# Kernel optimization log

Hardware: AMD Instinct MI355X
Metric: run time of the kernel (lower is better)

## Reference

```python
import jax, jax.numpy as jnp
import numpy as np

KS = 7
ITERS = 6
B, C, H, W = 2, 64, 256, 1216

_WM7 = [1,1,1,1,1,1,1,1,0,0,0,0,0,1,1,0,0,0,0,0,1,1,0,0,0,0,0,1,1,0,0,0,0,0,1,1,0,0,0,0,0,1,1,1,1,1,1,1,1]
_WM5 = [0,0,0,0,0,0,0,0,1,1,1,1,1,0,0,1,0,0,0,1,0,0,1,0,0,0,1,0,0,1,0,0,0,1,0,0,1,1,1,1,1,0,0,0,0,0,0,0,0]
_WM3 = [0,0,0,0,0,0,0,0,0,0,0,0,0,0,0,0,1,1,1,0,0,0,0,1,0,1,0,0,0,0,1,1,1,0,0,0,0,0,0,0,0,0,0,0,0,0,0,0,0]

# per 7x7 position t: which guide tensor (ring) and which channel within it
_SRC = []
_i7 = _i5 = _i3 = 0
for _t in range(KS * KS):
    if _WM7[_t]:
        _SRC.append(("7", _i7)); _i7 += 1
    elif _WM5[_t]:
        _SRC.append(("5", _i5)); _i5 += 1
    elif _WM3[_t]:
        _SRC.append(("3", _i3)); _i3 += 1
    else:
        _SRC.append(("1", 0))


def _convbn(x, w, s, b):
    # Conv2d(bias=False) + BatchNorm2d (inference) folded to per-channel scale/bias.
    y = jax.lax.conv_general_dilated(x, w, window_strides=(1, 1),
                                     padding=((1, 1), (1, 1)),
                                     dimension_numbers=("NCHW", "OIHW", "NCHW"))
    return y * s[None, :, None, None] + b[None, :, None, None]


def setup_inputs() -> dict:
    key = jax.random.key(0)
    ks = iter(jax.random.split(key, 64))
    def nrm(shape, scale=1.0):
        return jax.random.normal(next(ks), shape, jnp.float32) * scale
    def uni(shape):
        return jax.random.uniform(next(ks), shape, dtype=jnp.float32)
    inp = {
        "feature": nrm((B, C, H, W)),
        "d0": uni((B, 1, H, W)),
        "d00": nrm((B, 1, H, W)),  # ~half positive -> mixed valid_mask
    }
    layers = [("aff7", 24), ("aff5", 16), ("aff3", 8),
              ("att7", 6), ("att5", 6), ("att3", 6), ("att1", 6), ("mask", 6)]
    fan = 1.0 / np.sqrt(C * 9)
    for name, out in layers:
        inp["w_" + name] = nrm((out, C, 3, 3), fan)
        inp["s_" + name] = uni((out,))
        inp["b_" + name] = nrm((out,), 0.1)
    return inp


def reference(feature, d0, d00,
              w_aff7, s_aff7, b_aff7, w_aff5, s_aff5, b_aff5, w_aff3, s_aff3, b_aff3,
              w_att7, s_att7, b_att7, w_att5, s_att5, b_att5, w_att3, s_att3, b_att3,
              w_att1, s_att1, b_att1, w_mask, s_mask, b_mask):
    valid = (d00 > 0).astype(d00.dtype)
    mask_all = jax.nn.sigmoid(_convbn(feature, w_mask, s_mask, b_mask)) * valid
    aff7 = _convbn(feature, w_aff7, s_aff7, b_aff7)  # [B,24,H,W]
    aff5 = _convbn(feature, w_aff5, s_aff5, b_aff5)  # [B,16,H,W]
    aff3 = _convbn(feature, w_aff3, s_aff3, b_aff3)  # [B, 8,H,W]
    att7 = jax.nn.sigmoid(_convbn(feature, w_att7, s_att7, b_att7))
    att5 = jax.nn.sigmoid(_convbn(feature, w_att5, s_att5, b_att5))
    att3 = jax.nn.sigmoid(_convbn(feature, w_att3, s_att3, b_att3))
    att1 = jax.nn.sigmoid(_convbn(feature, w_att1, s_att1, b_att1))

    dt = d0
    for it in range(ITERS):
        mask = mask_all[:, it:it + 1]
        g7 = att7[:, it:it + 1] * aff7
        g5 = att5[:, it:it + 1] * aff5
        g3 = att3[:, it:it + 1] * aff3
        g1 = att1[:, it:it + 1]
        denom = (jnp.sum(jnp.abs(g7), 1, keepdims=True)
                 + jnp.sum(jnp.abs(g5), 1, keepdims=True)
                 + jnp.sum(jnp.abs(g3), 1, keepdims=True)
                 + jnp.abs(g1))
        g7, g5, g3, g1 = g7 / denom, g5 / denom, g3 / denom, g1 / denom
        g0 = 1.0 - (jnp.sum(g7, 1, keepdims=True) + jnp.sum(g5, 1, keepdims=True)
                    + jnp.sum(g3, 1, keepdims=True) + g1)
        guides = {"7": g7, "5": g5, "3": g3, "1": g1}
        # scatter ring guides into full 49-channel 7x7 layout
        G = jnp.concatenate([guides[k][:, i:i + 1] for k, i in _SRC], axis=1)  # [B,49,H,W]
        # weighted neighbor gather: out(p) = sum_t G_t(p+off_t) * dt(p+off_t)
        P = G * dt  # [B,49,H,W]
        Pp = jnp.pad(P, ((0, 0), (0, 0), (3, 3), (3, 3)))
        acc = jnp.zeros_like(dt)
        for t in range(KS * KS):
            i, j = t // KS, t % KS
            acc = acc + Pp[:, t:t + 1, 6 - i:6 - i + H, 6 - j:6 - j + W]
        dt = acc + g0 * d0
        dt = mask * d00 + (1.0 - mask) * dt
    return dt
```

## Files before the change

kernel.cpp:

```cpp
#include <hip/hip_runtime.h>
#include <hip/hip_fp16.h>
#include <stdint.h>

#define HH 256
#define WW 1216
#define BB 2
#define CC 64
#define IPIX (HH*WW)
#define NPIX (BB*IPIX)
#define PW 1280
#define PH 262
#define PPIX (PH*PW)
#define PLSTRIDE (BB*PPIX)
#define XOFF 32

typedef __attribute__((ext_vector_type(8))) __bf16 bf16x8;
typedef __attribute__((ext_vector_type(4))) __bf16 bf16x4;
typedef __attribute__((ext_vector_type(4))) float floatx4;
typedef __attribute__((ext_vector_type(4))) _Float16 half4;

__device__ __forceinline__ float sigm(float x) { return 1.f / (1.f + __expf(-x)); }

constexpr int LSTART_H[9] = {0,24,40,48,54,60,66,72,78};

constexpr int PLANE[49] = {
  0, 1, 2, 3, 4, 5, 6,
  7,24,25,26,27,28, 8,
  9,29,40,41,42,30,10,
 11,31,43,-1,44,32,12,
 13,33,45,46,47,34,14,
 15,35,36,37,38,39,16,
 17,18,19,20,21,22,23};
constexpr int KCLS[49] = {
 0,0,0,0,0,0,0,
 0,1,1,1,1,1,0,
 0,1,2,2,2,1,0,
 0,1,2,3,2,1,0,
 0,1,2,2,2,1,0,
 0,1,1,1,1,1,0,
 0,0,0,0,0,0,0};
constexpr int TAPNC[48] = {
  0,1,2,3,4,5,6,7,8,9,10,11,12,13,14,15,16,17,18,19,20,21,22,23,
  25,26,27,28,29,30,31,32,33,34,35,36,37,38,39,40,41,42,43,44,45,46,47,48};

struct WPtrs {
    const float* w[8];
    const float* s[8];
    const float* b[8];
};

__global__ void k_pack(WPtrs wp, __bf16* __restrict__ wpk,
                       float* __restrict__ s_all, float* __restrict__ b_all) {
    int idx = blockIdx.x * blockDim.x + threadIdx.x;
    if (idx < 18 * 5 * 64) {
        int kk = idx / (5 * 64);
        int r = idx - kk * 5 * 64;
        int t = r >> 6, lane = r & 63;
        int m = t * 16 + (lane & 15);
        int L = 0, o = 0;
        bool valid_m = (m < 78);
        if (valid_m) {
            for (int i = 0; i < 8; i++) if (m >= LSTART_H[i]) { L = i; o = m - LSTART_H[i]; }
        }
        __bf16 vals[8];
        for (int j = 0; j < 8; j++) {
            int k = kk * 32 + ((lane >> 4) * 8) + j;
            int tap = k >> 6, c = k & 63;
            float w = valid_m ? wp.w[L][(o * 64 + c) * 9 + tap] : 0.f;
            vals[j] = (__bf16)w;
        }
        for (int j = 0; j < 8; j++) wpk[(size_t)idx * 8 + j] = vals[j];
    }
    if (idx < 80) {
        int m = idx;
        float sv = 0.f, bv = 0.f;
        if (m < 78) {
            int L = 0, o = 0;
            for (int i = 0; i < 8; i++) if (m >= LSTART_H[i]) { L = i; o = m - LSTART_H[i]; }
            sv = wp.s[L][o]; bv = wp.b[L][o];
        }
        s_all[m] = sv; b_all[m] = bv;
    }
}

__global__ void k_zero_pad(__bf16* __restrict__ aff_p) {
    const int perPB = 6 * PW + 256 * 16;
    int idx = blockIdx.x * blockDim.x + threadIdx.x;
    int total = 48 * BB * perPB;
    if (idx >= total) return;
    int pbi = idx / perPB;
    int e = idx - pbi * perPB;
    int plane = pbi >> 1, b = pbi & 1;
    int r, c;
    if (e < 6 * PW) {
        int rr = e / PW; c = e - rr * PW;
        r = (rr < 3) ? rr : (259 + rr - 3);
    } else {
        int j = e - 6 * PW;
        r = 3 + (j >> 4);
        int c16 = j & 15;
        c = (c16 < 8) ? (24 + c16) : (1248 + c16 - 8);
    }
    aff_p[(size_t)plane * PLSTRIDE + (size_t)b * PPIX + r * PW + c] = (__bf16)0.f;
}

__global__ __launch_bounds__(256) void k_cvt(const float* __restrict__ feat,
                                             __bf16* __restrict__ fpk) {
    const int x = blockIdx.x * 64 + (threadIdx.x & 63);
    const int half = threadIdx.x >> 6;
    const int y = blockIdx.y, b = blockIdx.z;
    const float* fb = feat + (size_t)b * CC * IPIX + (size_t)y * WW + x;
    __bf16* op = fpk + ((size_t)(b * IPIX + y * WW + x) << 6);
#pragma unroll
    for (int h = 0; h < 2; h++) {
        const int cg = half + h * 4;
        bf16x8 pk;
#pragma unroll
        for (int j = 0; j < 8; j++) pk[j] = (__bf16)fb[(size_t)(cg * 8 + j) * IPIX];
        *(bf16x8*)(op + cg * 8) = pk;
    }
}

__global__ __launch_bounds__(256, 4) void k_conv(const __bf16* __restrict__ fpk,
        const float* __restrict__ d00, const __bf16* __restrict__ wpk,
        const float* __restrict__ s_all, const float* __restrict__ b_all,
        __bf16* __restrict__ aff_p, __bf16* __restrict__ attp, __bf16* __restrict__ maskp,
        float* __restrict__ stp) {
    __shared__ __bf16 sh[6 * 34 * 72];
    __shared__ __bf16 wlds[2 * 2560];
    const int tid = threadIdx.x;
    int flat = blockIdx.x + 38 * (blockIdx.y + 64 * blockIdx.z);
    int nf = (flat & 7) * 608 + (flat >> 3);
    int bx = nf % 38; int r2 = nf / 38;
    const int x0 = bx * 32, y0 = (r2 & 63) * 4, b = r2 >> 6;

    {
        bf16x8 w0 = *(const bf16x8*)(wpk + (size_t)tid * 8);
        *(bf16x8*)(wlds + tid * 8) = w0;
        if (tid < 64) {
            bf16x8 w1 = *(const bf16x8*)(wpk + 2048 + (size_t)tid * 8);
            *(bf16x8*)(wlds + 2048 + tid * 8) = w1;
        }
    }
    for (int idx = tid; idx < 204 * 8; idx += 256) {
        int cg = idx & 7, pos = idx >> 3;
        int row = pos / 34, x = pos - row * 34;
        int gy = y0 + row - 1, gx = x0 + x - 1;
        bf16x8 pk;
#pragma unroll
        for (int j = 0; j < 8; j++) pk[j] = (__bf16)0.f;
        if (gy >= 0 && gy < HH && gx >= 0 && gx < WW)
            pk = *(const bf16x8*)(fpk + ((size_t)(b * IPIX + gy * WW + gx) << 6) + cg * 8);
        *(bf16x8*)(sh + pos * 72 + cg * 8) = pk;
    }
    __syncthreads();

    const int wave = tid >> 6, lane = tid & 63;
    const int n = lane & 15, g = lane >> 4;

    floatx4 acc[5][2];
#pragma unroll
    for (int t = 0; t < 5; t++)
#pragma unroll
        for (int q = 0; q < 2; q++) acc[t][q] = (floatx4)(0.f);

#pragma unroll
    for (int kk = 0; kk < 18; kk++) {
        bf16x8 wt0, wt1;
        if (kk < 17) {
            wt0 = *(const bf16x8*)(wpk + (size_t)(kk + 1) * 2560 + tid * 8);
            if (tid < 64) wt1 = *(const bf16x8*)(wpk + (size_t)(kk + 1) * 2560 + 2048 + tid * 8);
        }
        const int tap = kk >> 1;
        const int dy = tap / 3 - 1, dx = tap % 3 - 1;
        const int c0 = (kk & 1) * 32 + g * 8;
        bf16x8 bfr[2];
        const int rowb = wave + 1 + dy;
        const int colb = 1 + dx + n;
#pragma unroll
        for (int q = 0; q < 2; q++)
            bfr[q] = *(const bf16x8*)(sh + ((rowb * 34) + colb + q * 16) * 72 + c0);
        bf16x8 afr[5];
        const __bf16* wb = wlds + (kk & 1) * 2560 + lane * 8;
#pragma unroll
        for (int t = 0; t < 5; t++) afr[t] = *(const bf16x8*)(wb + t * 512);
#pragma unroll
        for (int t = 0; t < 5; t++)
#pragma unroll
            for (int q = 0; q < 2; q++)
                acc[t][q] = __builtin_amdgcn_mfma_f32_16x16x32_bf16(afr[t], bfr[q], acc[t][q], 0, 0, 0);
        if (kk < 17) {
            *(bf16x8*)(wlds + ((kk + 1) & 1) * 2560 + tid * 8) = wt0;
            if (tid < 64) *(bf16x8*)(wlds + ((kk + 1) & 1) * 2560 + 2048 + tid * 8) = wt1;
        }
        __syncthreads();
    }

    const int pix_base = b * IPIX + (y0 + wave) * WW + x0 + n;
    float p7[2] = {0,0}, t7[2] = {0,0};
    float p5[2] = {0,0}, t5[2] = {0,0};
    float p3[2] = {0,0}, t3[2] = {0,0};

#pragma unroll
    for (int t = 0; t < 5; t++) {
        const floatx4 sv = *(const floatx4*)(s_all + t * 16 + 4 * g);
        const floatx4 bv = *(const floatx4*)(b_all + t * 16 + 4 * g);
#pragma unroll
        for (int q = 0; q < 2; q++) {
#pragma unroll
            for (int reg = 0; reg < 4; reg++) {
                const int m = t * 16 + 4 * g + reg;
                const float v = fmaf(acc[t][q][reg], sv[reg], bv[reg]);
                if (m < 24)                { p7[q] += fabsf(v); t7[q] += v; }
                else if (m < 40)           { p5[q] += fabsf(v); t5[q] += v; }
                else if (m < 48)           { p3[q] += fabsf(v); t3[q] += v; }
                const float outv = (m < 48) ? v : sigm(v);
                sh[m * 132 + wave * 32 + n + q * 16] = (__bf16)outv;
            }
        }
    }
#pragma unroll
    for (int q = 0; q < 2; q++) {
        p7[q] += __shfl_xor(p7[q], 16); p7[q] += __shfl_xor(p7[q], 32);
        t7[q] += __shfl_xor(t7[q], 16); t7[q] += __shfl_xor(t7[q], 32);
        p5[q] += __shfl_xor(p5[q], 16); p5[q] += __shfl_xor(p5[q], 32);
        t5[q] += __shfl_xor(t5[q], 16); t5[q] += __shfl_xor(t5[q], 32);
        p3[q] += __shfl_xor(p3[q], 16); p3[q] += __shfl_xor(p3[q], 32);
        t3[q] += __shfl_xor(t3[q], 16); t3[q] += __shfl_xor(t3[q], 32);
    }
    if (g == 0) {
#pragma unroll
        for (int q = 0; q < 2; q++) {
            const int pixq = pix_base + q * 16;
            floatx4 s0 = {p7[q], p5[q], p3[q], t7[q]};
            floatx4 s1 = {t5[q], t3[q], 0.f, 0.f};
            *(floatx4*)(stp + (size_t)pixq * 8)     = s0;
            *(floatx4*)(stp + (size_t)pixq * 8 + 4) = s1;
        }
    }
    __syncthreads();

    const int px = tid & 127;
    const int grp = tid >> 7;
    const int prow = px >> 5, pcol = px & 31;
    const size_t ppx = (size_t)b * PPIX + (y0 + prow + 3) * PW + (x0 + pcol + XOFF);
    const int pix = b * IPIX + (y0 + prow) * WW + x0 + pcol;
#pragma unroll
    for (int m = 0; m < 48; m += 2) {
        aff_p[(size_t)(m + grp) * PLSTRIDE + ppx] = sh[(m + grp) * 132 + px];
    }
    const float d00v = d00[pix];
    const float valid = (d00v > 0.f) ? 1.f : 0.f;
#pragma unroll
    for (int j = 0; j < 6; j += 2) {
        const int it = j + grp;
        bf16x4 av = { sh[(48 + it) * 132 + px], sh[(54 + it) * 132 + px],
                      sh[(60 + it) * 132 + px], sh[(66 + it) * 132 + px] };
        *(bf16x4*)(attp + ((size_t)it * NPIX + pix) * 4) = av;
        maskp[(size_t)it * NPIX + pix] = (__bf16)((float)sh[(72 + it) * 132 + px] * valid);
    }
}

__global__ __launch_bounds__(256) void k_rg(const __bf16* __restrict__ attp,
        const float* __restrict__ stp, const float* __restrict__ d0,
        _Float16* __restrict__ rp, float* __restrict__ gd) {
    int g = blockIdx.x * blockDim.x + threadIdx.x;
    if (g >= NPIX) return;
    const floatx4 s0 = *(const floatx4*)(stp + (size_t)g * 8);
    const floatx4 s1 = *(const floatx4*)(stp + (size_t)g * 8 + 4);
    const float S7 = s0[0], S5 = s0[1], S3 = s0[2], T7 = s0[3], T5 = s1[0], T3 = s1[1];
    const float d0v = d0[g];
#pragma unroll
    for (int it = 0; it < 6; it++) {
        bf16x4 a = *(const bf16x4*)(attp + ((size_t)it * NPIX + g) * 4);
        float a7 = (float)a[0], a5 = (float)a[1], a3 = (float)a[2], a1 = (float)a[3];
        float denom = a7 * S7 + a5 * S5 + a3 * S3 + a1;
        float inv = 1.f / denom;
        float r7 = a7 * inv, r5 = a5 * inv, r3 = a3 * inv, r1 = a1 * inv;
        float g0 = 1.f - (r7 * T7 + r5 * T5 + r3 * T3 + r1);
        half4 rv = {(_Float16)r7, (_Float16)r5, (_Float16)r3, (_Float16)r1};
        *(half4*)(rp + ((size_t)it * NPIX + g) * 4) = rv;
        gd[(size_t)it * NPIX + g] = g0 * d0v;
    }
}

__global__ __launch_bounds__(256) void k_iter(const _Float16* __restrict__ rp,
        const float* __restrict__ gd, const float* __restrict__ dt,
        const __bf16* __restrict__ aff_p, const __bf16* __restrict__ maskp,
        const float* __restrict__ d00,
        float* __restrict__ dtn, int it) {
    __shared__ float sp[5][14 * 38];
    const int tid = threadIdx.x;
    const int tx = tid & 31, ty = tid >> 5;
    int flat = blockIdx.x + 38 * (blockIdx.y + 32 * blockIdx.z);
    int nf = (flat & 7) * 304 + (flat >> 3);
    int bx = nf % 38; int r2 = nf / 38;
    const int x0 = bx * 32, y0 = (r2 & 31) * 8, b = r2 >> 5;
    const int ib = b * IPIX;

    for (int idx = tid; idx < 14 * 38; idx += 256) {
        int r = idx / 38, col = idx - r * 38;
        int gy = y0 + r - 3, gx = x0 + col - 3;
        float v7 = 0.f, v5 = 0.f, v3 = 0.f, v1 = 0.f, vb = 0.f;
        if (gy >= 0 && gy < HH && gx >= 0 && gx < WW) {
            int q = ib + gy * WW + gx;
            half4 rv = *(const half4*)(rp + ((size_t)it * NPIX + q) * 4);
            float dtv = dt[q];
            v7 = (float)rv[0] * dtv; v5 = (float)rv[1] * dtv;
            v3 = (float)rv[2] * dtv; v1 = (float)rv[3] * dtv;
            vb = gd[(size_t)it * NPIX + q];
        }
        sp[0][idx] = v7; sp[1][idx] = v5; sp[2][idx] = v3; sp[3][idx] = v1; sp[4][idx] = vb;
    }
    __syncthreads();

    const int y = y0 + ty, x = x0 + tx;
    const int pix = ib + y * WW + x;
    const __bf16* ap = aff_p + (size_t)b * PPIX + (y + 3) * PW + (x + XOFF);

    float acc0 = sp[4][(ty + 3) * 38 + (tx + 3)] + sp[3][(ty + 3) * 38 + (tx + 3)];
    float acc1 = 0.f, acc2 = 0.f, acc3 = 0.f;
#pragma unroll
    for (int bt = 0; bt < 6; bt++) {
        float a8[8];
#pragma unroll
        for (int j = 0; j < 8; j++) {
            const int t = TAPNC[bt * 8 + j];
            const int dy = 3 - t / 7, dx = 3 - (t % 7);
            a8[j] = (float)ap[(ptrdiff_t)PLANE[t] * PLSTRIDE + dy * PW + dx];
        }
#pragma unroll
        for (int j = 0; j < 8; j++) {
            const int t = TAPNC[bt * 8 + j];
            const int dy = 3 - t / 7, dx = 3 - (t % 7);
            const float pv = sp[KCLS[t]][(ty + dy + 3) * 38 + (tx + dx + 3)];
            switch (j & 3) {
                case 0: acc0 = fmaf(a8[j], pv, acc0); break;
                case 1: acc1 = fmaf(a8[j], pv, acc1); break;
                case 2: acc2 = fmaf(a8[j], pv, acc2); break;
                default: acc3 = fmaf(a8[j], pv, acc3); break;
            }
        }
    }
    float acc = (acc0 + acc1) + (acc2 + acc3);
    float m = (float)maskp[(size_t)it * NPIX + pix];
    float dtv = m * d00[pix] + (1.f - m) * acc;
    dtn[pix] = dtv;
}

extern "C" void kernel_launch(void* const* d_in, const int* in_sizes, int n_in,
                              void* d_out, int out_size, void* d_ws, size_t ws_size,
                              hipStream_t stream) {
    const float* feat = (const float*)d_in[0];
    const float* d0   = (const float*)d_in[1];
    const float* d00  = (const float*)d_in[2];
    WPtrs wp;
    for (int l = 0; l < 8; l++) {
        wp.w[l] = (const float*)d_in[3 + 3 * l];
        wp.s[l] = (const float*)d_in[4 + 3 * l];
        wp.b[l] = (const float*)d_in[5 + 3 * l];
    }
    __bf16*   wsb   = (__bf16*)d_ws;
    __bf16*   aff_p = wsb;
    __bf16*   attp  = aff_p + (size_t)48 * PLSTRIDE;
    __bf16*   msk_b = attp + (size_t)24 * NPIX;
    float*    stp   = (float*)(msk_b + (size_t)6 * NPIX);
    float*    dtA   = stp + (size_t)8 * NPIX;
    __bf16*   wpk   = (__bf16*)(dtA + (size_t)NPIX);
    float*    s_all = (float*)(wpk + 18 * 5 * 64 * 8);
    float*    b_all = s_all + 80;
    char*     X     = (char*)(b_all + 80);
    __bf16*   fpk   = (__bf16*)X;
    _Float16* rp    = (_Float16*)X;
    float*    gd    = (float*)(X + (size_t)24 * NPIX * 2);
    float*    dtB   = (float*)d_out;

    hipLaunchKernelGGL(k_pack, dim3(23), dim3(256), 0, stream, wp, wpk, s_all, b_all);
    hipLaunchKernelGGL(k_zero_pad, dim3((48 * BB * (6 * PW + 256 * 16) + 255) / 256), dim3(256),
                       0, stream, aff_p);
    hipLaunchKernelGGL(k_cvt, dim3(WW / 64, HH, BB), dim3(256), 0, stream, feat, fpk);
    hipLaunchKernelGGL(k_conv, dim3(38, 64, 2), dim3(256), 0, stream,
                       fpk, d00, wpk, s_all, b_all, aff_p, attp, msk_b, stp);
    hipLaunchKernelGGL(k_rg, dim3(NPIX / 256), dim3(256), 0, stream,
                       attp, stp, d0, rp, gd);
    const float* cur = d0;
    for (int it = 0; it < 6; ++it) {
        float* nxt = (it & 1) ? dtB : dtA;
        if (it == 5) nxt = dtB;
        hipLaunchKernelGGL(k_iter, dim3(38, 32, 2), dim3(256), 0, stream,
                           rp, gd, cur, aff_p, msk_b, d00, nxt, it);
        cur = nxt;
    }
}
```

Baseline: 523.6 us.

## Store affinities pixel-major and scatter iteration taps via LDS atomics

The 48 affinity planes are now written in a pixel-interleaved layout (48 bf16 per pixel) instead of padded planar buffers, so the zero-pad kernel goes away. The iteration kernel changes from a gather to a scatter: each source pixel reads its 48 contiguous affinities and atomically adds the weighted contributions into an LDS accumulation tile, on a taller 16-row tile. The conv kernel drops its LDS double-buffered weight staging and per-step barriers, reading weights directly from global/L2, and raises its occupancy hint. The trade-offs are heavy LDS atomic traffic (49 atomics per source pixel, with halo redundancy) and weight loads that now go to cache instead of LDS.

```diff
diff --git a/kernel.cpp b/kernel.cpp
--- a/kernel.cpp
+++ b/kernel.cpp
@@ -8,11 +8,6 @@
 #define CC 64
 #define IPIX (HH*WW)
 #define NPIX (BB*IPIX)
-#define PW 1280
-#define PH 262
-#define PPIX (PH*PW)
-#define PLSTRIDE (BB*PPIX)
-#define XOFF 32
 
 typedef __attribute__((ext_vector_type(8))) __bf16 bf16x8;
 typedef __attribute__((ext_vector_type(4))) __bf16 bf16x4;
@@ -49,6 +44,10 @@
     const float* b[8];
 };
 
+__device__ __forceinline__ void lds_fadd(float* p, float v) {
+    __hip_atomic_fetch_add(p, v, __ATOMIC_RELAXED, __HIP_MEMORY_SCOPE_WORKGROUP);
+}
+
 __global__ void k_pack(WPtrs wp, __bf16* __restrict__ wpk,
                        float* __restrict__ s_all, float* __restrict__ b_all) {
     int idx = blockIdx.x * blockDim.x + threadIdx.x;
@@ -83,27 +82,6 @@
     }
 }
 
-__global__ void k_zero_pad(__bf16* __restrict__ aff_p) {
-    const int perPB = 6 * PW + 256 * 16;
-    int idx = blockIdx.x * blockDim.x + threadIdx.x;
-    int total = 48 * BB * perPB;
-    if (idx >= total) return;
-    int pbi = idx / perPB;
-    int e = idx - pbi * perPB;
-    int plane = pbi >> 1, b = pbi & 1;
-    int r, c;
-    if (e < 6 * PW) {
-        int rr = e / PW; c = e - rr * PW;
-        r = (rr < 3) ? rr : (259 + rr - 3);
-    } else {
-        int j = e - 6 * PW;
-        r = 3 + (j >> 4);
-        int c16 = j & 15;
-        c = (c16 < 8) ? (24 + c16) : (1248 + c16 - 8);
-    }
-    aff_p[(size_t)plane * PLSTRIDE + (size_t)b * PPIX + r * PW + c] = (__bf16)0.f;
-}
-
 __global__ __launch_bounds__(256) void k_cvt(const float* __restrict__ feat,
                                              __bf16* __restrict__ fpk) {
     const int x = blockIdx.x * 64 + (threadIdx.x & 63);
@@ -121,27 +99,18 @@
     }
 }
 
-__global__ __launch_bounds__(256, 4) void k_conv(const __bf16* __restrict__ fpk,
+__global__ __launch_bounds__(256, 5) void k_conv(const __bf16* __restrict__ fpk,
         const float* __restrict__ d00, const __bf16* __restrict__ wpk,
         const float* __restrict__ s_all, const float* __restrict__ b_all,
-        __bf16* __restrict__ aff_p, __bf16* __restrict__ attp, __bf16* __restrict__ maskp,
+        __bf16* __restrict__ afx, __bf16* __restrict__ attp, __bf16* __restrict__ maskp,
         float* __restrict__ stp) {
     __shared__ __bf16 sh[6 * 34 * 72];
-    __shared__ __bf16 wlds[2 * 2560];
     const int tid = threadIdx.x;
     int flat = blockIdx.x + 38 * (blockIdx.y + 64 * blockIdx.z);
     int nf = (flat & 7) * 608 + (flat >> 3);
     int bx = nf % 38; int r2 = nf / 38;
     const int x0 = bx * 32, y0 = (r2 & 63) * 4, b = r2 >> 6;
 
-    {
-        bf16x8 w0 = *(const bf16x8*)(wpk + (size_t)tid * 8);
-        *(bf16x8*)(wlds + tid * 8) = w0;
-        if (tid < 64) {
-            bf16x8 w1 = *(const bf16x8*)(wpk + 2048 + (size_t)tid * 8);
-            *(bf16x8*)(wlds + 2048 + tid * 8) = w1;
-        }
-    }
     for (int idx = tid; idx < 204 * 8; idx += 256) {
         int cg = idx & 7, pos = idx >> 3;
         int row = pos / 34, x = pos - row * 34;
@@ -166,11 +135,6 @@
 
 #pragma unroll
     for (int kk = 0; kk < 18; kk++) {
-        bf16x8 wt0, wt1;
-        if (kk < 17) {
-            wt0 = *(const bf16x8*)(wpk + (size_t)(kk + 1) * 2560 + tid * 8);
-            if (tid < 64) wt1 = *(const bf16x8*)(wpk + (size_t)(kk + 1) * 2560 + 2048 + tid * 8);
-        }
         const int tap = kk >> 1;
         const int dy = tap / 3 - 1, dx = tap % 3 - 1;
         const int c0 = (kk & 1) * 32 + g * 8;
@@ -180,8 +144,8 @@
 #pragma unroll
         for (int q = 0; q < 2; q++)
             bfr[q] = *(const bf16x8*)(sh + ((rowb * 34) + colb + q * 16) * 72 + c0);
+        const __bf16* wb = wpk + (size_t)kk * 2560 + lane * 8;
         bf16x8 afr[5];
-        const __bf16* wb = wlds + (kk & 1) * 2560 + lane * 8;
 #pragma unroll
         for (int t = 0; t < 5; t++) afr[t] = *(const bf16x8*)(wb + t * 512);
 #pragma unroll
@@ -189,12 +153,8 @@
 #pragma unroll
             for (int q = 0; q < 2; q++)
                 acc[t][q] = __builtin_amdgcn_mfma_f32_16x16x32_bf16(afr[t], bfr[q], acc[t][q], 0, 0, 0);
-        if (kk < 17) {
-            *(bf16x8*)(wlds + ((kk + 1) & 1) * 2560 + tid * 8) = wt0;
-            if (tid < 64) *(bf16x8*)(wlds + ((kk + 1) & 1) * 2560 + 2048 + tid * 8) = wt1;
-        }
-        __syncthreads();
-    }
+    }
+    __syncthreads();
 
     const int pix_base = b * IPIX + (y0 + wave) * WW + x0 + n;
     float p7[2] = {0,0}, t7[2] = {0,0};
@@ -240,15 +200,27 @@
     }
     __syncthreads();
 
+    {
+        const int pxi = tid >> 1;
+        const int hf = tid & 1;
+        const int prow2 = pxi >> 5, pcol2 = pxi & 31;
+        const int pix2 = b * IPIX + (y0 + prow2) * WW + x0 + pcol2;
+#pragma unroll
+        for (int k = 0; k < 3; k++) {
+            bf16x8 v;
+#pragma unroll
+            for (int e = 0; e < 8; e++) {
+                const int jj = hf * 24 + k * 8 + e;
+                v[e] = sh[PLANE[TAPNC[jj]] * 132 + pxi];
+            }
+            *(bf16x8*)(afx + (size_t)pix2 * 48 + hf * 24 + k * 8) = v;
+        }
+    }
+
     const int px = tid & 127;
     const int grp = tid >> 7;
     const int prow = px >> 5, pcol = px & 31;
-    const size_t ppx = (size_t)b * PPIX + (y0 + prow + 3) * PW + (x0 + pcol + XOFF);
     const int pix = b * IPIX + (y0 + prow) * WW + x0 + pcol;
-#pragma unroll
-    for (int m = 0; m < 48; m += 2) {
-        aff_p[(size_t)(m + grp) * PLSTRIDE + ppx] = sh[(m + grp) * 132 + px];
-    }
     const float d00v = d00[pix];
     const float valid = (d00v > 0.f) ? 1.f : 0.f;
 #pragma unroll
@@ -286,66 +258,67 @@
 
 __global__ __launch_bounds__(256) void k_iter(const _Float16* __restrict__ rp,
         const float* __restrict__ gd, const float* __restrict__ dt,
-        const __bf16* __restrict__ aff_p, const __bf16* __restrict__ maskp,
+        const __bf16* __restrict__ afx, const __bf16* __restrict__ maskp,
         const float* __restrict__ d00,
         float* __restrict__ dtn, int it) {
-    __shared__ float sp[5][14 * 38];
+    __shared__ float accs[28 * 44];
     const int tid = threadIdx.x;
+    int flat = blockIdx.x + 38 * (blockIdx.y + 16 * blockIdx.z);
+    int nf = (flat & 7) * 152 + (flat >> 3);
+    int bx = nf % 38; int r2 = nf / 38;
+    const int x0 = bx * 32, y0 = (r2 & 15) * 16, b = r2 >> 4;
+    const int ib = b * IPIX;
+
+    for (int idx = tid; idx < 28 * 44; idx += 256) accs[idx] = 0.f;
+    __syncthreads();
+
+    for (int idx = tid; idx < 22 * 38; idx += 256) {
+        const int ly = idx / 38, lx = idx - ly * 38;
+        const int gy = y0 + ly - 3, gx = x0 + lx - 3;
+        if (gy >= 0 && gy < HH && gx >= 0 && gx < WW) {
+            const int q = ib + gy * WW + gx;
+            const half4 rv = *(const half4*)(rp + ((size_t)it * NPIX + q) * 4);
+            const float dtv = dt[q];
+            const float gdv = gd[(size_t)it * NPIX + q];
+            float rc[4];
+            rc[0] = (float)rv[0] * dtv; rc[1] = (float)rv[1] * dtv;
+            rc[2] = (float)rv[2] * dtv; rc[3] = (float)rv[3] * dtv;
+            bf16x8 A0 = *(const bf16x8*)(afx + (size_t)q * 48);
+            bf16x8 A1 = *(const bf16x8*)(afx + (size_t)q * 48 + 8);
+            bf16x8 A2 = *(const bf16x8*)(afx + (size_t)q * 48 + 16);
+            bf16x8 A3 = *(const bf16x8*)(afx + (size_t)q * 48 + 24);
+            bf16x8 A4 = *(const bf16x8*)(afx + (size_t)q * 48 + 32);
+            bf16x8 A5 = *(const bf16x8*)(afx + (size_t)q * 48 + 40);
+            float* abase = accs + ly * 44 + lx;
+            lds_fadd(abase + 3 * 44 + 3, rc[3] + gdv);
+#pragma unroll
+            for (int jj = 0; jj < 48; jj++) {
+                const int t = TAPNC[jj];
+                const int i = t / 7, j = t % 7;
+                float av;
+                switch (jj >> 3) {
+                    case 0: av = (float)A0[jj & 7]; break;
+                    case 1: av = (float)A1[jj & 7]; break;
+                    case 2: av = (float)A2[jj & 7]; break;
+                    case 3: av = (float)A3[jj & 7]; break;
+                    case 4: av = (float)A4[jj & 7]; break;
+                    default: av = (float)A5[jj & 7]; break;
+                }
+                lds_fadd(abase + i * 44 + j, av * rc[KCLS[t]]);
+            }
+        }
+    }
+    __syncthreads();
+
     const int tx = tid & 31, ty = tid >> 5;
-    int flat = blockIdx.x + 38 * (blockIdx.y + 32 * blockIdx.z);
-    int nf = (flat & 7) * 304 + (flat >> 3);
-    int bx = nf % 38; int r2 = nf / 38;
-    const int x0 = bx * 32, y0 = (r2 & 31) * 8, b = r2 >> 5;
-    const int ib = b * IPIX;
-
-    for (int idx = tid; idx < 14 * 38; idx += 256) {
-        int r = idx / 38, col = idx - r * 38;
-        int gy = y0 + r - 3, gx = x0 + col - 3;
-        float v7 = 0.f, v5 = 0.f, v3 = 0.f, v1 = 0.f, vb = 0.f;
-        if (gy >= 0 && gy < HH && gx >= 0 && gx < WW) {
-            int q = ib + gy * WW + gx;
-            half4 rv = *(const half4*)(rp + ((size_t)it * NPIX + q) * 4);
-            float dtv = dt[q];
-            v7 = (float)rv[0] * dtv; v5 = (float)rv[1] * dtv;
-            v3 = (float)rv[2] * dtv; v1 = (float)rv[3] * dtv;
-            vb = gd[(size_t)it * NPIX + q];
-        }
-        sp[0][idx] = v7; sp[1][idx] = v5; sp[2][idx] = v3; sp[3][idx] = v1; sp[4][idx] = vb;
-    }
-    __syncthreads();
-
-    const int y = y0 + ty, x = x0 + tx;
-    const int pix = ib + y * WW + x;
-    const __bf16* ap = aff_p + (size_t)b * PPIX + (y + 3) * PW + (x + XOFF);
-
-    float acc0 = sp[4][(ty + 3) * 38 + (tx + 3)] + sp[3][(ty + 3) * 38 + (tx + 3)];
-    float acc1 = 0.f, acc2 = 0.f, acc3 = 0.f;
-#pragma unroll
-    for (int bt = 0; bt < 6; bt++) {
-        float a8[8];
-#pragma unroll
-        for (int j = 0; j < 8; j++) {
-            const int t = TAPNC[bt * 8 + j];
-            const int dy = 3 - t / 7, dx = 3 - (t % 7);
-            a8[j] = (float)ap[(ptrdiff_t)PLANE[t] * PLSTRIDE + dy * PW + dx];
-        }
-#pragma unroll
-        for (int j = 0; j < 8; j++) {
-            const int t = TAPNC[bt * 8 + j];
-            const int dy = 3 - t / 7, dx = 3 - (t % 7);
-            const float pv = sp[KCLS[t]][(ty + dy + 3) * 38 + (tx + dx + 3)];
-            switch (j & 3) {
-                case 0: acc0 = fmaf(a8[j], pv, acc0); break;
-                case 1: acc1 = fmaf(a8[j], pv, acc1); break;
-                case 2: acc2 = fmaf(a8[j], pv, acc2); break;
-                default: acc3 = fmaf(a8[j], pv, acc3); break;
-            }
-        }
-    }
-    float acc = (acc0 + acc1) + (acc2 + acc3);
-    float m = (float)maskp[(size_t)it * NPIX + pix];
-    float dtv = m * d00[pix] + (1.f - m) * acc;
-    dtn[pix] = dtv;
+#pragma unroll
+    for (int r = 0; r < 16; r += 8) {
+        const int oy = ty + r;
+        const int pix = ib + (y0 + oy) * WW + (x0 + tx);
+        const float acc = accs[(oy + 6) * 44 + (tx + 6)];
+        const float m = (float)maskp[(size_t)it * NPIX + pix];
+        dtn[pix] = m * d00[pix] + (1.f - m) * acc;
+    }
 }
 
 extern "C" void kernel_launch(void* const* d_in, const int* in_sizes, int n_in,
@@ -361,8 +334,8 @@
         wp.b[l] = (const float*)d_in[5 + 3 * l];
     }
     __bf16*   wsb   = (__bf16*)d_ws;
-    __bf16*   aff_p = wsb;
-    __bf16*   attp  = aff_p + (size_t)48 * PLSTRIDE;
+    __bf16*   afx   = wsb;
+    __bf16*   attp  = afx + (size_t)48 * NPIX;
     __bf16*   msk_b = attp + (size_t)24 * NPIX;
     float*    stp   = (float*)(msk_b + (size_t)6 * NPIX);
     float*    dtA   = stp + (size_t)8 * NPIX;
@@ -376,19 +349,17 @@
     float*    dtB   = (float*)d_out;
 
     hipLaunchKernelGGL(k_pack, dim3(23), dim3(256), 0, stream, wp, wpk, s_all, b_all);
-    hipLaunchKernelGGL(k_zero_pad, dim3((48 * BB * (6 * PW + 256 * 16) + 255) / 256), dim3(256),
-                       0, stream, aff_p);
     hipLaunchKernelGGL(k_cvt, dim3(WW / 64, HH, BB), dim3(256), 0, stream, feat, fpk);
     hipLaunchKernelGGL(k_conv, dim3(38, 64, 2), dim3(256), 0, stream,
-                       fpk, d00, wpk, s_all, b_all, aff_p, attp, msk_b, stp);
+                       fpk, d00, wpk, s_all, b_all, afx, attp, msk_b, stp);
     hipLaunchKernelGGL(k_rg, dim3(NPIX / 256), dim3(256), 0, stream,
                        attp, stp, d0, rp, gd);
     const float* cur = d0;
     for (int it = 0; it < 6; ++it) {
         float* nxt = (it & 1) ? dtB : dtA;
         if (it == 5) nxt = dtB;
-        hipLaunchKernelGGL(k_iter, dim3(38, 32, 2), dim3(256), 0, stream,
-                           rp, gd, cur, aff_p, msk_b, d00, nxt, it);
+        hipLaunchKernelGGL(k_iter, dim3(38, 16, 2), dim3(256), 0, stream,
+                           rp, gd, cur, afx, msk_b, d00, nxt, it);
         cur = nxt;
     }
 }
```

Result: slower. 1.997 ms (+281.4%).

## Fuse pairs of propagation iterations into one kernel with halo recompute

Applied to the files above, without the earlier changes.

Replaces six per-iteration launches with three launches that each run two propagation steps. A wider halo of the weighted input is staged in shared memory, and the intermediate iteration is recomputed over a 22x38 region held in LDS, so the intermediate depth never goes to global memory. Tiles grow to 16 rows, and the gd term is folded into the fourth plane so there are four planes instead of five. The cost is redundant halo compute and extra affinity loads for the intermediate region, plus more shared memory per block, which may lower occupancy.

```diff
diff --git a/kernel.cpp b/kernel.cpp
--- a/kernel.cpp
+++ b/kernel.cpp
@@ -284,68 +284,121 @@
     }
 }
 
-__global__ __launch_bounds__(256) void k_iter(const _Float16* __restrict__ rp,
-        const float* __restrict__ gd, const float* __restrict__ dt,
+#define R0W 44
+#define R0N (28 * 44)
+#define R1W 38
+#define R1N (22 * 38)
+__global__ __launch_bounds__(256) void k_iter2(const _Float16* __restrict__ rp,
+        const float* __restrict__ gd, const float* __restrict__ src,
         const __bf16* __restrict__ aff_p, const __bf16* __restrict__ maskp,
         const float* __restrict__ d00,
-        float* __restrict__ dtn, int it) {
-    __shared__ float sp[5][14 * 38];
+        float* __restrict__ dtn, int itA) {
+    __shared__ float P0[4][R0N];
+    __shared__ float P1[4][R1N];
+    const int itB = itA + 1;
     const int tid = threadIdx.x;
+    int flat = blockIdx.x + 38 * (blockIdx.y + 16 * blockIdx.z);
+    int nf = (flat & 7) * 152 + (flat >> 3);
+    int bx = nf % 38; int r2 = nf / 38;
+    const int x0 = bx * 32, y0 = (r2 & 15) * 16, b = r2 >> 4;
+    const int ib = b * IPIX;
+
+    for (int idx = tid; idx < R0N; idx += 256) {
+        const int r = idx / R0W, c = idx - r * R0W;
+        const int gy = y0 + r - 6, gx = x0 + c - 6;
+        float c0 = 0.f, c1 = 0.f, c2 = 0.f, c3 = 0.f;
+        if (gy >= 0 && gy < HH && gx >= 0 && gx < WW) {
+            const int q = ib + gy * WW + gx;
+            const half4 rv = *(const half4*)(rp + ((size_t)itA * NPIX + q) * 4);
+            const float dtv = src[q];
+            const float gdv = gd[(size_t)itA * NPIX + q];
+            c0 = (float)rv[0] * dtv; c1 = (float)rv[1] * dtv;
+            c2 = (float)rv[2] * dtv; c3 = (float)rv[3] * dtv + gdv;
+        }
+        P0[0][idx] = c0; P0[1][idx] = c1; P0[2][idx] = c2; P0[3][idx] = c3;
+    }
+    __syncthreads();
+
+    for (int idx = tid; idx < R1N; idx += 256) {
+        const int r = idx / R1W, c = idx - r * R1W;
+        const int gy = y0 + r - 3, gx = x0 + c - 3;
+        float o0 = 0.f, o1 = 0.f, o2 = 0.f, o3 = 0.f;
+        if (gy >= 0 && gy < HH && gx >= 0 && gx < WW) {
+            const int q = ib + gy * WW + gx;
+            const __bf16* ap = aff_p + (size_t)b * PPIX + (gy + 3) * PW + (gx + XOFF);
+            const int cb = (r + 3) * R0W + (c + 3);
+            float a0 = P0[3][cb];
+            float a1 = 0.f, a2 = 0.f, a3 = 0.f;
+#pragma unroll
+            for (int bt = 0; bt < 6; bt++) {
+                float a8[8];
+#pragma unroll
+                for (int j = 0; j < 8; j++) {
+                    const int t = TAPNC[bt * 8 + j];
+                    const int dy = 3 - t / 7, dx = 3 - (t % 7);
+                    a8[j] = (float)ap[(ptrdiff_t)PLANE[t] * PLSTRIDE + dy * PW + dx];
+                }
+#pragma unroll
+                for (int j = 0; j < 8; j++) {
+                    const int t = TAPNC[bt * 8 + j];
+                    const int dy = 3 - t / 7, dx = 3 - (t % 7);
+                    const float pv = P0[KCLS[t]][cb + dy * R0W + dx];
+                    switch (j & 3) {
+                        case 0: a0 = fmaf(a8[j], pv, a0); break;
+                        case 1: a1 = fmaf(a8[j], pv, a1); break;
+                        case 2: a2 = fmaf(a8[j], pv, a2); break;
+                        default: a3 = fmaf(a8[j], pv, a3); break;
+                    }
+                }
+            }
+            const float acc = (a0 + a1) + (a2 + a3);
+            const float m = (float)maskp[(size_t)itA * NPIX + q];
+            const float dtA = m * d00[q] + (1.f - m) * acc;
+            const half4 rv = *(const half4*)(rp + ((size_t)itB * NPIX + q) * 4);
+            const float gdv = gd[(size_t)itB * NPIX + q];
+            o0 = (float)rv[0] * dtA; o1 = (float)rv[1] * dtA;
+            o2 = (float)rv[2] * dtA; o3 = (float)rv[3] * dtA + gdv;
+        }
+        P1[0][idx] = o0; P1[1][idx] = o1; P1[2][idx] = o2; P1[3][idx] = o3;
+    }
+    __syncthreads();
+
     const int tx = tid & 31, ty = tid >> 5;
-    int flat = blockIdx.x + 38 * (blockIdx.y + 32 * blockIdx.z);
-    int nf = (flat & 7) * 304 + (flat >> 3);
-    int bx = nf % 38; int r2 = nf / 38;
-    const int x0 = bx * 32, y0 = (r2 & 31) * 8, b = r2 >> 5;
-    const int ib = b * IPIX;
-
-    for (int idx = tid; idx < 14 * 38; idx += 256) {
-        int r = idx / 38, col = idx - r * 38;
-        int gy = y0 + r - 3, gx = x0 + col - 3;
-        float v7 = 0.f, v5 = 0.f, v3 = 0.f, v1 = 0.f, vb = 0.f;
-        if (gy >= 0 && gy < HH && gx >= 0 && gx < WW) {
-            int q = ib + gy * WW + gx;
-            half4 rv = *(const half4*)(rp + ((size_t)it * NPIX + q) * 4);
-            float dtv = dt[q];
-            v7 = (float)rv[0] * dtv; v5 = (float)rv[1] * dtv;
-            v3 = (float)rv[2] * dtv; v1 = (float)rv[3] * dtv;
-            vb = gd[(size_t)it * NPIX + q];
-        }
-        sp[0][idx] = v7; sp[1][idx] = v5; sp[2][idx] = v3; sp[3][idx] = v1; sp[4][idx] = vb;
-    }
-    __syncthreads();
-
-    const int y = y0 + ty, x = x0 + tx;
-    const int pix = ib + y * WW + x;
-    const __bf16* ap = aff_p + (size_t)b * PPIX + (y + 3) * PW + (x + XOFF);
-
-    float acc0 = sp[4][(ty + 3) * 38 + (tx + 3)] + sp[3][(ty + 3) * 38 + (tx + 3)];
-    float acc1 = 0.f, acc2 = 0.f, acc3 = 0.f;
-#pragma unroll
-    for (int bt = 0; bt < 6; bt++) {
-        float a8[8];
-#pragma unroll
-        for (int j = 0; j < 8; j++) {
-            const int t = TAPNC[bt * 8 + j];
-            const int dy = 3 - t / 7, dx = 3 - (t % 7);
-            a8[j] = (float)ap[(ptrdiff_t)PLANE[t] * PLSTRIDE + dy * PW + dx];
-        }
-#pragma unroll
-        for (int j = 0; j < 8; j++) {
-            const int t = TAPNC[bt * 8 + j];
-            const int dy = 3 - t / 7, dx = 3 - (t % 7);
-            const float pv = sp[KCLS[t]][(ty + dy + 3) * 38 + (tx + dx + 3)];
-            switch (j & 3) {
-                case 0: acc0 = fmaf(a8[j], pv, acc0); break;
-                case 1: acc1 = fmaf(a8[j], pv, acc1); break;
-                case 2: acc2 = fmaf(a8[j], pv, acc2); break;
-                default: acc3 = fmaf(a8[j], pv, acc3); break;
+#pragma unroll
+    for (int rr = 0; rr < 16; rr += 8) {
+        const int oy = ty + rr;
+        const int gy = y0 + oy, gx = x0 + tx;
+        const int pix = ib + gy * WW + gx;
+        const __bf16* ap = aff_p + (size_t)b * PPIX + (gy + 3) * PW + (gx + XOFF);
+        const int cb = (oy + 3) * R1W + (tx + 3);
+        float a0 = P1[3][cb];
+        float a1 = 0.f, a2 = 0.f, a3 = 0.f;
+#pragma unroll
+        for (int bt = 0; bt < 6; bt++) {
+            float a8[8];
+#pragma unroll
+            for (int j = 0; j < 8; j++) {
+                const int t = TAPNC[bt * 8 + j];
+                const int dy = 3 - t / 7, dx = 3 - (t % 7);
+                a8[j] = (float)ap[(ptrdiff_t)PLANE[t] * PLSTRIDE + dy * PW + dx];
             }
-        }
-    }
-    float acc = (acc0 + acc1) + (acc2 + acc3);
-    float m = (float)maskp[(size_t)it * NPIX + pix];
-    float dtv = m * d00[pix] + (1.f - m) * acc;
-    dtn[pix] = dtv;
+#pragma unroll
+            for (int j = 0; j < 8; j++) {
+                const int t = TAPNC[bt * 8 + j];
+                const int dy = 3 - t / 7, dx = 3 - (t % 7);
+                const float pv = P1[KCLS[t]][cb + dy * R1W + dx];
+                switch (j & 3) {
+                    case 0: a0 = fmaf(a8[j], pv, a0); break;
+                    case 1: a1 = fmaf(a8[j], pv, a1); break;
+                    case 2: a2 = fmaf(a8[j], pv, a2); break;
+                    default: a3 = fmaf(a8[j], pv, a3); break;
+                }
+            }
+        }
+        const float acc = (a0 + a1) + (a2 + a3);
+        const float m = (float)maskp[(size_t)itB * NPIX + pix];
+        dtn[pix] = m * d00[pix] + (1.f - m) * acc;
+    }
 }
 
 extern "C" void kernel_launch(void* const* d_in, const int* in_sizes, int n_in,
@@ -366,14 +419,14 @@
     __bf16*   msk_b = attp + (size_t)24 * NPIX;
     float*    stp   = (float*)(msk_b + (size_t)6 * NPIX);
     float*    dtA   = stp + (size_t)8 * NPIX;
-    __bf16*   wpk   = (__bf16*)(dtA + (size_t)NPIX);
+    float*    dtC   = dtA + (size_t)NPIX;
+    __bf16*   wpk   = (__bf16*)(dtC + (size_t)NPIX);
     float*    s_all = (float*)(wpk + 18 * 5 * 64 * 8);
     float*    b_all = s_all + 80;
     char*     X     = (char*)(b_all + 80);
     __bf16*   fpk   = (__bf16*)X;
     _Float16* rp    = (_Float16*)X;
     float*    gd    = (float*)(X + (size_t)24 * NPIX * 2);
-    float*    dtB   = (float*)d_out;
 
     hipLaunchKernelGGL(k_pack, dim3(23), dim3(256), 0, stream, wp, wpk, s_all, b_all);
     hipLaunchKernelGGL(k_zero_pad, dim3((48 * BB * (6 * PW + 256 * 16) + 255) / 256), dim3(256),
@@ -383,12 +436,10 @@
                        fpk, d00, wpk, s_all, b_all, aff_p, attp, msk_b, stp);
     hipLaunchKernelGGL(k_rg, dim3(NPIX / 256), dim3(256), 0, stream,
                        attp, stp, d0, rp, gd);
-    const float* cur = d0;
-    for (int it = 0; it < 6; ++it) {
-        float* nxt = (it & 1) ? dtB : dtA;
-        if (it == 5) nxt = dtB;
-        hipLaunchKernelGGL(k_iter, dim3(38, 32, 2), dim3(256), 0, stream,
-                           rp, gd, cur, aff_p, msk_b, d00, nxt, it);
-        cur = nxt;
-    }
-}
+    hipLaunchKernelGGL(k_iter2, dim3(38, 16, 2), dim3(256), 0, stream,
+                       rp, gd, d0, aff_p, msk_b, d00, dtA, 0);
+    hipLaunchKernelGGL(k_iter2, dim3(38, 16, 2), dim3(256), 0, stream,
+                       rp, gd, dtA, aff_p, msk_b, d00, dtC, 2);
+    hipLaunchKernelGGL(k_iter2, dim3(38, 16, 2), dim3(256), 0, stream,
+                       rp, gd, dtC, aff_p, msk_b, d00, (float*)d_out, 4);
+}
```

Measured after the change: 540.6 us. 1.03x slower.
